# Kernel optimization log

Hardware: AMD Instinct MI355X
Metric: run time of the kernel (lower is better)

## Reference

```python
import jax, jax.numpy as jnp
import numpy as np

DIM = 1024
HEADS = 16
HEAD_DIM = DIM // HEADS
NEG = -1e30
EPS = 1e-5


def _linear(x, w, b):
    # torch nn.Linear: y = x @ W^T + b, W: [out, in]
    return jnp.einsum('bnd,od->bno', x, w) + b


def _mha(x, ctx, wq, bq, wk, bk, wv, bv, wo, bo, mask):
    B, N, D = x.shape
    M = ctx.shape[1]
    q = _linear(x, wq, bq).reshape(B, N, HEADS, HEAD_DIM).transpose(0, 2, 1, 3)
    k = _linear(ctx, wk, bk).reshape(B, M, HEADS, HEAD_DIM).transpose(0, 2, 1, 3)
    v = _linear(ctx, wv, bv).reshape(B, M, HEADS, HEAD_DIM).transpose(0, 2, 1, 3)
    scores = jnp.einsum('bhqd,bhkd->bhqk', q, k) / np.sqrt(HEAD_DIM).astype(np.float32)
    if mask is not None:
        scores = jnp.where(mask == 0, NEG, scores)
    attn = jax.nn.softmax(scores, axis=-1)  # dropout = identity (eval mode)
    out = jnp.einsum('bhqk,bhkd->bhqd', attn, v)
    out = out.transpose(0, 2, 1, 3).reshape(B, N, D)
    return _linear(out, wo, bo)


def _ln(x, g, b):
    mu = jnp.mean(x, axis=-1, keepdims=True)
    var = jnp.mean(jnp.square(x - mu), axis=-1, keepdims=True)
    return (x - mu) * jax.lax.rsqrt(var + EPS) * g + b


def setup_inputs() -> dict:
    key = jax.random.key(0)
    ks = jax.random.split(key, 24)
    B, N, M = 2, 2048, 1024
    s = 0.02
    d = {
        'x': jax.random.normal(ks[0], (B, N, DIM), jnp.float32),
        'memory': jax.random.normal(ks[1], (B, M, DIM), jnp.float32),
        'mask': jnp.tril(jnp.ones((N, N), jnp.int32))[None, None],
    }
    i = 2
    for p in ['sa', 'ca']:
        for nm in ['q', 'k', 'v', 'o']:
            d[f'{p}_w{nm}'] = jax.random.normal(ks[i], (DIM, DIM), jnp.float32) * s; i += 1
            d[f'{p}_b{nm}'] = jnp.zeros((DIM,), jnp.float32)
    d['ff_w1'] = jax.random.normal(ks[i], (4 * DIM, DIM), jnp.float32) * s; i += 1
    d['ff_b1'] = jnp.zeros((4 * DIM,), jnp.float32)
    d['ff_w2'] = jax.random.normal(ks[i], (DIM, 4 * DIM), jnp.float32) * s; i += 1
    d['ff_b2'] = jnp.zeros((DIM,), jnp.float32)
    for j in (1, 2, 3):
        d[f'ln{j}_g'] = jnp.ones((DIM,), jnp.float32)
        d[f'ln{j}_b'] = jnp.zeros((DIM,), jnp.float32)
    return d


def reference(x, memory, mask,
              sa_wq, sa_bq, sa_wk, sa_bk, sa_wv, sa_bv, sa_wo, sa_bo,
              ca_wq, ca_bq, ca_wk, ca_bk, ca_wv, ca_bv, ca_wo, ca_bo,
              ff_w1, ff_b1, ff_w2, ff_b2,
              ln1_g, ln1_b, ln2_g, ln2_b, ln3_g, ln3_b):
    x = _ln(x + _mha(x, x, sa_wq, sa_bq, sa_wk, sa_bk, sa_wv, sa_bv, sa_wo, sa_bo, mask), ln1_g, ln1_b)
    x = _ln(x + _mha(x, memory, ca_wq, ca_bq, ca_wk, ca_bk, ca_wv, ca_bv, ca_wo, ca_bo, None), ln2_g, ln2_b)
    h = jax.nn.relu(_linear(x, ff_w1, ff_b1))  # dropout = identity (eval)
    x = _ln(x + _linear(h, ff_w2, ff_b2), ln3_g, ln3_b)
    return x
```

## Files before the change

### kernel.cpp

```cpp
#include <hip/hip_runtime.h>


typedef __attribute__((ext_vector_type(8))) short bf16x8;
typedef __attribute__((ext_vector_type(4))) float f32x4;

__device__ __forceinline__ unsigned short f2bf(float f) {
    union { float f; unsigned int u; } v; v.f = f;
    unsigned int r = v.u + 0x7fffu + ((v.u >> 16) & 1u);
    return (unsigned short)(r >> 16);
}
__device__ __forceinline__ float bf2f(unsigned short u) {
    union { unsigned int u; float f; } v; v.u = (unsigned int)u << 16;
    return v.f;
}
__device__ __forceinline__ unsigned int bftrunc(float f) {
    union { float f; unsigned int u; } v; v.f = f;
    return v.u >> 16;
}

struct ConvArgs {
    const float* src[12];
    unsigned short* dst[12];
    int blk_ofs[13];
    int n4[12];
    const float* bq; const float* bk; const float* bv;
    const float* ck; const float* cv;
    float* bqkv; float* bkvc;
};
__global__ __launch_bounds__(256) void conv_multi(ConvArgs a)
{
    int bid = blockIdx.x;
    if (bid >= a.blk_ofs[12]) {
        int i = (bid - a.blk_ofs[12]) * 256 + threadIdx.x;
        if (i < 1024)       a.bqkv[i] = a.bq[i];
        else if (i < 2048)  a.bqkv[i] = a.bk[i - 1024];
        else if (i < 3072)  a.bqkv[i] = a.bv[i - 2048];
        else if (i < 4096)  a.bkvc[i - 3072] = a.ck[i - 3072];
        else if (i < 5120)  a.bkvc[i - 3072] = a.cv[i - 4096];
        return;
    }
    int s = 0;
#pragma unroll
    for (int t = 0; t < 12; ++t) if (bid >= a.blk_ofs[t + 1]) s = t + 1;
    int i = (bid - a.blk_ofs[s]) * 256 + threadIdx.x;
    if (i >= a.n4[s]) return;
    float4 v = ((const float4*)a.src[s])[i];
    ushort4 o;
    o.x = f2bf(v.x); o.y = f2bf(v.y); o.z = f2bf(v.z); o.w = f2bf(v.w);
    ((ushort4*)a.dst[s])[i] = o;
}

template<int TM, int TN, int EPI, int SK>
__device__ __forceinline__ void gemm_body(
    unsigned short (*As)[64], unsigned short (*Bs)[64],
    const unsigned short* __restrict__ A, const unsigned short* __restrict__ W,
    const float* __restrict__ bias, unsigned short* __restrict__ out,
    int K, int Ncols, long slice_stride, int bid, int gx, int zslice)
{
    constexpr int AI = TM / 32;
    constexpr int BJ = TN / 32;

    const int tid  = threadIdx.x;
    const int lane = tid & 63;
    const int wave = tid >> 6;
    const int qd   = lane >> 4;
    const int l15  = lane & 15;
    const int wm   = (wave >> 1) * (TM / 2);
    const int wn   = (wave & 1) * (TN / 2);

    const int gpg = 8 * gx;
    const long m0 = (long)((bid / gpg) * 8 + (bid & 7)) * TM;
    const long n0 = (long)((bid % gpg) >> 3) * TN;

    f32x4 acc[AI][BJ] = {};

    const int srow = lane >> 3;
    const int scol = (((lane & 7) ^ srow)) * 8;
    const unsigned short* Ag = A + (m0 + wave * (8 * AI) + srow) * (long)K + scol;
    const unsigned short* Wg = W + (n0 + wave * (8 * BJ) + srow) * (long)K + scol;

    const int ksl   = K / SK;
    const int kbase = (SK > 1) ? zslice * ksl : 0;

    for (int k0 = kbase; k0 < kbase + ksl; k0 += 64) {
#pragma unroll
        for (int c = 0; c < AI; ++c)
            __builtin_amdgcn_global_load_lds(
                (const __attribute__((address_space(1))) unsigned int*)(Ag + (long)c * 8 * K + k0),
                (__attribute__((address_space(3))) unsigned int*)((char*)&As[0][0] + (wave * AI + c) * 1024),
                16, 0, 0);
#pragma unroll
        for (int c = 0; c < BJ; ++c)
            __builtin_amdgcn_global_load_lds(
                (const __attribute__((address_space(1))) unsigned int*)(Wg + (long)c * 8 * K + k0),
                (__attribute__((address_space(3))) unsigned int*)((char*)&Bs[0][0] + (wave * BJ + c) * 1024),
                16, 0, 0);
        __syncthreads();
#pragma unroll
        for (int kk = 0; kk < 64; kk += 32) {
            const int pg = ((((kk >> 3) + qd)) ^ (l15 & 7)) * 8;
            bf16x8 af[AI], bw[BJ];
#pragma unroll
            for (int i = 0; i < AI; ++i)
                af[i] = *(const bf16x8*)&As[wm + i * 16 + l15][pg];
#pragma unroll
            for (int j = 0; j < BJ; ++j)
                bw[j] = *(const bf16x8*)&Bs[wn + j * 16 + l15][pg];
#pragma unroll
            for (int i = 0; i < AI; ++i)
#pragma unroll
                for (int j = 0; j < BJ; ++j)
                    acc[i][j] = __builtin_amdgcn_mfma_f32_16x16x32_bf16(
                        af[i], bw[j], acc[i][j], 0, 0, 0);
        }
        __syncthreads();
    }

    unsigned short* op = out + ((SK > 1) ? (long)zslice * slice_stride : 0);
#pragma unroll
    for (int j = 0; j < BJ; ++j) {
        long col = n0 + wn + j * 16 + l15;
        float bv = (SK == 1 || zslice == 0) ? bias[col] : 0.f;
#pragma unroll
        for (int i = 0; i < AI; ++i) {
#pragma unroll
            for (int r = 0; r < 4; ++r) {
                long row = m0 + wm + i * 16 + qd * 4 + r;
                float v = acc[i][j][r] + bv;
                if (EPI == 1) v = (v > 0.f) ? v : 0.f;
                op[row * Ncols + col] = f2bf(v);
            }
        }
    }
}

template<int TM, int TN, int EPI, int SK>
__global__ __launch_bounds__(256) void gemm_bt(
    const unsigned short* __restrict__ A, const unsigned short* __restrict__ W,
    const float* __restrict__ bias, unsigned short* __restrict__ out,
    int K, int Ncols, long slice_stride)
{
    __shared__ unsigned short As[TM][64];
    __shared__ unsigned short Bs[TN][64];
    const int bid = blockIdx.y * gridDim.x + blockIdx.x;
    gemm_body<TM, TN, EPI, SK>(As, Bs, A, W, bias, out, K, Ncols, slice_stride,
                               bid, gridDim.x, (int)blockIdx.z);
}

template<int EPI, int SK>
__device__ __forceinline__ void gemm8_body(
    unsigned short* Ab, unsigned short* Bb,
    const unsigned short* __restrict__ A, const unsigned short* __restrict__ W,
    const float* __restrict__ bias, unsigned short* __restrict__ out,
    int K, int Ncols, long slice_stride, int mb, int nb, int zslice)
{
    const int tid  = threadIdx.x;
    const int lane = tid & 63;
    const int wave = tid >> 6;
    const int qd   = lane >> 4;
    const int l15  = lane & 15;
    const int wm   = (wave >> 2) * 128;
    const int wn   = (wave & 3) * 64;

    const long m0 = (long)mb * 256;
    const long n0 = (long)nb * 256;

    const int ksl   = K / SK;
    const int kbase = (SK > 1) ? zslice * ksl : 0;
    const int NG    = ksl / 64;

    f32x4 acc[8][4] = {};

    const int srow = tid >> 3;
    const int sgrp = ((tid & 7) ^ (srow & 7)) * 8;
    const unsigned short* Ag = A + (m0 + srow) * (long)K + kbase + sgrp;
    const unsigned short* Wg = W + (n0 + srow) * (long)K + kbase + sgrp;

    auto stA = [&](int db, int r0, int kt) {
        __builtin_amdgcn_global_load_lds(
            (const __attribute__((address_space(1))) unsigned int*)(Ag + (long)r0 * K + kt * 64),
            (__attribute__((address_space(3))) unsigned int*)(Ab + db * 16384 + r0 * 64 + wave * 512),
            16, 0, 0);
    };
    auto stB = [&](int db, int r0, int kt) {
        __builtin_amdgcn_global_load_lds(
            (const __attribute__((address_space(1))) unsigned int*)(Wg + (long)r0 * K + kt * 64),
            (__attribute__((address_space(3))) unsigned int*)(Bb + db * 16384 + r0 * 64 + wave * 512),
            16, 0, 0);
    };
    auto rdA = [&](int db, int row, int kk) -> bf16x8 {
        const int p = (((kk << 2) + qd) ^ (l15 & 7)) << 3;
        return *(const bf16x8*)(Ab + db * 16384 + row * 64 + p);
    };
    auto rdB = [&](int db, int row, int kk) -> bf16x8 {
        const int p = (((kk << 2) + qd) ^ (l15 & 7)) << 3;
        return *(const bf16x8*)(Bb + db * 16384 + row * 64 + p);
    };

#pragma unroll
    for (int h = 0; h < 4; ++h) stA(0, h * 64, 0);
#pragma unroll
    for (int h = 0; h < 4; ++h) stB(0, h * 64, 0);
    if (NG > 1) {
#pragma unroll
        for (int h = 0; h < 4; ++h) stB(1, h * 64, 1);
        stA(1, 0, 1); stA(1, 128, 1);
        asm volatile("s_waitcnt vmcnt(6)" ::: "memory");
    } else {
        asm volatile("s_waitcnt vmcnt(0)" ::: "memory");
    }
    __builtin_amdgcn_s_barrier();

    for (int g = 0; g < NG; ++g) {
        const int db = g & 1, ob = db ^ 1;
        bf16x8 af[4][2], bw[4][2];

        if (g + 1 < NG) { stA(ob, 64, g + 1); stA(ob, 192, g + 1); }

#pragma unroll
        for (int i = 0; i < 4; ++i)
#pragma unroll
            for (int kk = 0; kk < 2; ++kk)
                af[i][kk] = rdA(db, wm + i * 16 + l15, kk);
#pragma unroll
        for (int j = 0; j < 4; ++j)
#pragma unroll
            for (int kk = 0; kk < 2; ++kk)
                bw[j][kk] = rdB(db, wn + j * 16 + l15, kk);
        __builtin_amdgcn_s_setprio(1);
#pragma unroll
        for (int i = 0; i < 4; ++i)
#pragma unroll
            for (int j = 0; j < 4; ++j) {
                acc[i][j] = __builtin_amdgcn_mfma_f32_16x16x32_bf16(af[i][0], bw[j][0], acc[i][j], 0, 0, 0);
                acc[i][j] = __builtin_amdgcn_mfma_f32_16x16x32_bf16(af[i][1], bw[j][1], acc[i][j], 0, 0, 0);
            }
        __builtin_amdgcn_s_setprio(0);
        __builtin_amdgcn_s_barrier();

        if (g + 2 < NG) {
#pragma unroll
            for (int h = 0; h < 4; ++h) stB(db, h * 64, g + 2);
            stA(db, 0, g + 2); stA(db, 128, g + 2);
        }

#pragma unroll
        for (int i = 0; i < 4; ++i)
#pragma unroll
            for (int kk = 0; kk < 2; ++kk)
                af[i][kk] = rdA(db, wm + 64 + i * 16 + l15, kk);
        __builtin_amdgcn_s_setprio(1);
#pragma unroll
        for (int i = 0; i < 4; ++i)
#pragma unroll
            for (int j = 0; j < 4; ++j) {
                acc[4 + i][j] = __builtin_amdgcn_mfma_f32_16x16x32_bf16(af[i][0], bw[j][0], acc[4 + i][j], 0, 0, 0);
                acc[4 + i][j] = __builtin_amdgcn_mfma_f32_16x16x32_bf16(af[i][1], bw[j][1], acc[4 + i][j], 0, 0, 0);
            }
        __builtin_amdgcn_s_setprio(0);

        if (g + 2 < NG)      { asm volatile("s_waitcnt vmcnt(6)" ::: "memory"); }
        else if (g + 1 < NG) { asm volatile("s_waitcnt vmcnt(0)" ::: "memory"); }
        __builtin_amdgcn_s_barrier();
    }

    unsigned short* op = out + ((SK > 1) ? (long)zslice * slice_stride : 0);
#pragma unroll
    for (int j = 0; j < 4; ++j) {
        long col = n0 + wn + j * 16 + l15;
        float bv = (SK == 1 || zslice == 0) ? bias[col] : 0.f;
#pragma unroll
        for (int i = 0; i < 8; ++i) {
#pragma unroll
            for (int r = 0; r < 4; ++r) {
                long row = m0 + wm + (i >> 2) * 64 + (i & 3) * 16 + qd * 4 + r;
                float v = acc[i][j][r] + bv;
                if (EPI == 1) v = (v > 0.f) ? v : 0.f;
                op[row * Ncols + col] = f2bf(v);
            }
        }
    }
}

template<int EPI, int SK, int MODE>
__global__ __launch_bounds__(512) void gemm8_bt(
    const unsigned short* __restrict__ A, const unsigned short* __restrict__ W,
    const float* __restrict__ bias, unsigned short* __restrict__ out,
    int K, int Ncols, long slice_stride)
{
    extern __shared__ unsigned short smem[];
    const int bid = blockIdx.x;
    const int x = bid & 7;
    const int s = bid >> 3;
    int mb, nb, z = 0;
    if (MODE == 1) {
        mb = (x >> 1) * 4 + (s & 3);
        nb = (x & 1) * 8 + (s >> 2);
    } else {
        z  = x >> 1;
        mb = (x & 1) * 8 + (s & 7);
        nb = s >> 3;
    }
    gemm8_body<EPI, SK>(smem, smem + 32768, A, W, bias, out, K, Ncols,
                        slice_stride, mb, nb, z);
}

__global__ __launch_bounds__(512) void gemm8_dual(
    const unsigned short* A0, const unsigned short* W0, const float* b0,
    unsigned short* o0, int K0, int N0,
    const unsigned short* A1, const unsigned short* W1, const float* b1,
    unsigned short* o1, int K1, int N1)
{
    extern __shared__ unsigned short smem[];
    const int bid = blockIdx.x;
    const int x = bid & 7;
    const int s = bid >> 3;
    if (s < 24) {
        const int mb = (x >> 1) * 4 + (s & 3);
        const int nb = (x & 1) * 6 + (s >> 2);
        gemm8_body<0, 1>(smem, smem + 32768, A0, W0, b0, o0, K0, N0, 0, mb, nb, 0);
    } else {
        const int t = s - 24;
        const int mb = (x >> 1) * 2 + (t & 1);
        const int nb = (x & 1) * 4 + (t >> 1);
        gemm8_body<0, 1>(smem, smem + 32768, A1, W1, b1, o1, K1, N1, 0, mb, nb, 0);
    }
}

__global__ __launch_bounds__(256) void attn_kernel(
    const unsigned short* __restrict__ Qb, int q_stride,
    const unsigned short* __restrict__ KVb, int kv_stride, int koff, int voff,
    unsigned short* __restrict__ O,
    int Nq, int Mk, int causal)
{
    __shared__ unsigned short Ks[64][64];
    __shared__ unsigned short Vs[64][64];
    __shared__ unsigned short Ps[4][16][64];

    const int tid  = threadIdx.x;
    const int lane = tid & 63;
    const int wave = tid >> 6;
    const int qd   = lane >> 4;
    const int l15  = lane & 15;
    const int l7   = l15 & 7;
    const int h    = blockIdx.y;
    const int b    = blockIdx.z;
    int jq = blockIdx.x;
    if (causal && (b & 1)) jq = gridDim.x - 1 - jq;
    const int q0 = jq * 64;
    const int tb = q0 + wave * 16;

    bf16x8 aq0, aq1;
    {
        const unsigned short* qp =
            Qb + (long)(b * Nq + tb + l15) * q_stride + h * 64 + qd * 8;
        aq0 = *(const bf16x8*)qp;
        aq1 = *(const bf16x8*)(qp + 32);
    }

    float lpart[4] = {};
    f32x4 oacc[4] = {};

    const int krow  = tid >> 3;
    const int kcol  = (tid & 7) * 8;
    const int kcolS = (((tid & 7) ^ (krow & 7))) * 8;
    const int vj   = tid & 31;
    const int va_k = (vj & 15) + ((vj & 16) << 1);
    const int vfg  = (tid >> 5) * 8;
    const int vpc  = (va_k & 15) * 4 + (va_k >> 4);

    const unsigned short* Kg = KVb + (long)b * Mk * kv_stride + koff + h * 64;
    const unsigned short* Vg = KVb + (long)b * Mk * kv_stride + voff + h * 64;

    bf16x8 kr0, kr1, vra, vrb;
    auto prefetch = [&](int k0) {
        kr0 = *(const bf16x8*)(Kg + (long)(k0 + krow) * kv_stride + kcol);
        kr1 = *(const bf16x8*)(Kg + (long)(k0 + krow + 32) * kv_stride + kcol);
        const unsigned short* v0 = Vg + (long)(k0 + va_k) * kv_stride + vfg;
        vra = *(const bf16x8*)v0;
        vrb = *(const bf16x8*)(v0 + 16 * kv_stride);
    };

    const int nk = causal ? (q0 + 64) : Mk;
    prefetch(0);
    const float SCL = 0.125f * 1.44269504f;

    for (int k0 = 0; k0 < nk; k0 += 64) {
        __syncthreads();
        *(bf16x8*)&Ks[krow][kcolS]      = kr0;
        *(bf16x8*)&Ks[krow + 32][kcolS] = kr1;
#pragma unroll
        for (int jf = 0; jf < 8; ++jf) {
            unsigned int d = (unsigned short)vra[jf] |
                             ((unsigned int)(unsigned short)vrb[jf] << 16);
            const int row = vfg + jf;
            *(unsigned int*)&Vs[row][vpc ^ ((row & 7) << 3)] = d;
        }
        if (k0 + 64 < nk) prefetch(k0 + 64);
        __syncthreads();

        if (!causal || (k0 <= tb + 15)) {
            bf16x8 bk[4][2];
#pragma unroll
            for (int kt = 0; kt < 4; ++kt)
#pragma unroll
                for (int c = 0; c < 2; ++c)
                    bk[kt][c] = *(const bf16x8*)&Ks[kt * 16 + l15][((c * 4 + qd) ^ l7) * 8];
            f32x4 s[4];
#pragma unroll
            for (int kt = 0; kt < 4; ++kt) {
                f32x4 z = {};
                z = __builtin_amdgcn_mfma_f32_16x16x32_bf16(aq0, bk[kt][0], z, 0, 0, 0);
                z = __builtin_amdgcn_mfma_f32_16x16x32_bf16(aq1, bk[kt][1], z, 0, 0, 0);
                s[kt] = z;
            }
            const bool needmask = causal && (k0 + 63 > tb);
#pragma unroll
            for (int r = 0; r < 4; ++r) {
                const int qg = tb + qd * 4 + r;
                float e[4];
#pragma unroll
                for (int kt = 0; kt < 4; ++kt) {
                    float ev = __builtin_amdgcn_exp2f(s[kt][r] * SCL);
                    if (needmask && (k0 + kt * 16 + l15 > qg)) ev = 0.f;
                    e[kt] = ev;
                }
                lpart[r] += (e[0] + e[1]) + (e[2] + e[3]);
                unsigned int lo = bftrunc(e[0]) | (bftrunc(e[1]) << 16);
                unsigned int hi = bftrunc(e[2]) | (bftrunc(e[3]) << 16);
                uint2 pk; pk.x = lo; pk.y = hi;
                const int prow = qd * 4 + r;
                *(uint2*)&Ps[wave][prow][(l15 * 4) ^ ((prow & 7) << 3)] = pk;
            }
            bf16x8 bv[4][2];
#pragma unroll
            for (int dt = 0; dt < 4; ++dt)
#pragma unroll
                for (int c = 0; c < 2; ++c)
                    bv[dt][c] = *(const bf16x8*)&Vs[dt * 16 + l15][((c * 4 + qd) ^ l7) * 8];
            bf16x8 ap0 = *(const bf16x8*)&Ps[wave][l15][(qd ^ l7) * 8];
            bf16x8 ap1 = *(const bf16x8*)&Ps[wave][l15][((4 + qd) ^ l7) * 8];
#pragma unroll
            for (int dt = 0; dt < 4; ++dt) {
                oacc[dt] = __builtin_amdgcn_mfma_f32_16x16x32_bf16(
                    ap0, bv[dt][0], oacc[dt], 0, 0, 0);
                oacc[dt] = __builtin_amdgcn_mfma_f32_16x16x32_bf16(
                    ap1, bv[dt][1], oacc[dt], 0, 0, 0);
            }
        }
    }

#pragma unroll
    for (int r = 0; r < 4; ++r) {
        float l = lpart[r];
        l += __shfl_xor(l, 1);
        l += __shfl_xor(l, 2);
        l += __shfl_xor(l, 4);
        l += __shfl_xor(l, 8);
        float inv = 1.f / l;
        long row = (long)(b * Nq + tb + qd * 4 + r);
#pragma unroll
        for (int dt = 0; dt < 4; ++dt)
            O[row * 1024 + h * 64 + dt * 16 + l15] = f2bf(oacc[dt][r] * inv);
    }
}

template<int ND, int RESBF>
__global__ __launch_bounds__(256) void ln_res_kernel(
    const void* __restrict__ res, const unsigned short* __restrict__ delta,
    long dstride, const float* __restrict__ g, const float* __restrict__ beta,
    float* __restrict__ yout, unsigned short* __restrict__ ybf)
{
    __shared__ float red[8];
    const int row = blockIdx.x;
    const int tid = threadIdx.x;
    const long base = (long)row * 1024 + tid * 4;
    float v0, v1, v2, v3;
    if (RESBF) {
        ushort4 a = *(const ushort4*)((const unsigned short*)res + base);
        v0 = bf2f(a.x); v1 = bf2f(a.y); v2 = bf2f(a.z); v3 = bf2f(a.w);
    } else {
        float4 a = *(const float4*)((const float*)res + base);
        v0 = a.x; v1 = a.y; v2 = a.z; v3 = a.w;
    }
#pragma unroll
    for (int t = 0; t < ND; ++t) {
        ushort4 d = *(const ushort4*)(delta + t * dstride + base);
        v0 += bf2f(d.x); v1 += bf2f(d.y); v2 += bf2f(d.z); v3 += bf2f(d.w);
    }
    float s  = v0 + v1 + v2 + v3;
    float ss = v0 * v0 + v1 * v1 + v2 * v2 + v3 * v3;
#pragma unroll
    for (int off = 1; off < 64; off <<= 1) {
        s  += __shfl_xor(s, off);
        ss += __shfl_xor(ss, off);
    }
    const int wave = tid >> 6;
    if ((tid & 63) == 0) { red[wave] = s; red[4 + wave] = ss; }
    __syncthreads();
    float st  = red[0] + red[1] + red[2] + red[3];
    float sst = red[4] + red[5] + red[6] + red[7];
    float mean = st * (1.f / 1024.f);
    float var  = sst * (1.f / 1024.f) - mean * mean;
    float inv  = rsqrtf(var + 1e-5f);
    const int c = tid * 4;
    float y0 = (v0 - mean) * inv * g[c + 0] + beta[c + 0];
    float y1 = (v1 - mean) * inv * g[c + 1] + beta[c + 1];
    float y2 = (v2 - mean) * inv * g[c + 2] + beta[c + 2];
    float y3 = (v3 - mean) * inv * g[c + 3] + beta[c + 3];
    if (yout) *(float4*)(yout + base) = make_float4(y0, y1, y2, y3);
    if (ybf) {
        ushort4 o;
        o.x = f2bf(y0); o.y = f2bf(y1); o.z = f2bf(y2); o.w = f2bf(y3);
        *(ushort4*)(ybf + base) = o;
    }
}

extern "C" void kernel_launch(void* const* d_in, const int* in_sizes, int n_in,
                              void* d_out, int out_size, void* d_ws, size_t ws_size,
                              hipStream_t stream)
{
    const int B = 2, N = 2048, M = 1024, D = 1024, FF = 4096;
    const int TN = B * N;
    const int TM = B * M;
    const size_t MB = 1024 * 1024;

    const float* x     = (const float*)d_in[0];
    const float* mem   = (const float*)d_in[1];
    const float* sa_wq = (const float*)d_in[3];  const float* sa_bq = (const float*)d_in[4];
    const float* sa_wk = (const float*)d_in[5];  const float* sa_bk = (const float*)d_in[6];
    const float* sa_wv = (const float*)d_in[7];  const float* sa_bv = (const float*)d_in[8];
    const float* sa_wo = (const float*)d_in[9];  const float* sa_bo = (const float*)d_in[10];
    const float* ca_wq = (const float*)d_in[11]; const float* ca_bq = (const float*)d_in[12];
    const float* ca_wk = (const float*)d_in[13]; const float* ca_bk = (const float*)d_in[14];
    const float* ca_wv = (const float*)d_in[15]; const float* ca_bv = (const float*)d_in[16];
    const float* ca_wo = (const float*)d_in[17]; const float* ca_bo = (const float*)d_in[18];
    const float* ff_w1 = (const float*)d_in[19]; const float* ff_b1 = (const float*)d_in[20];
    const float* ff_w2 = (const float*)d_in[21]; const float* ff_b2 = (const float*)d_in[22];
    const float* ln1_g = (const float*)d_in[23]; const float* ln1_b = (const float*)d_in[24];
    const float* ln2_g = (const float*)d_in[25]; const float* ln2_b = (const float*)d_in[26];
    const float* ln3_g = (const float*)d_in[27]; const float* ln3_b = (const float*)d_in[28];

    char* w = (char*)d_ws;
    size_t off = 0;
    auto alloc = [&](size_t bytes) -> char* {
        char* p = w + off; off += (bytes + 255) & ~(size_t)255; return p;
    };

    unsigned short* xb   = (unsigned short*)alloc((size_t)TN * D * 2);
    unsigned short* memb = (unsigned short*)alloc((size_t)TM * D * 2);
    unsigned short* wqkv = (unsigned short*)alloc((size_t)3 * D * D * 2);
    unsigned short* wos  = (unsigned short*)alloc((size_t)D * D * 2);
    unsigned short* wqc  = (unsigned short*)alloc((size_t)D * D * 2);
    unsigned short* wkvc = (unsigned short*)alloc((size_t)2 * D * D * 2);
    unsigned short* woc  = (unsigned short*)alloc((size_t)D * D * 2);
    unsigned short* w1b  = (unsigned short*)alloc((size_t)FF * D * 2);
    unsigned short* w2b  = (unsigned short*)alloc((size_t)D * FF * 2);
    char* big = alloc((size_t)80 * MB);
    unsigned short* qkv   = (unsigned short*)big;
    unsigned short* ab    = (unsigned short*)(big + 24 * MB);
    unsigned short* kvb   = (unsigned short*)(big + 32 * MB);
    unsigned short* qb    = (unsigned short*)(big + 40 * MB);
    unsigned short* hb    = (unsigned short*)big;
    unsigned short* tmpbf = (unsigned short*)(big + 48 * MB);
    const long      TSL   = (long)TN * D;
    float* bqkv = (float*)alloc((size_t)3 * D * 4);
    float* bkvc = (float*)alloc((size_t)2 * D * 4);

    ConvArgs ca;
    const float* srcs[12] = {x, mem, sa_wq, sa_wk, sa_wv, sa_wo,
                             ca_wq, ca_wk, ca_wv, ca_wo, ff_w1, ff_w2};
    unsigned short* dsts[12] = {xb, memb, wqkv, wqkv + (size_t)D * D,
                                wqkv + (size_t)2 * D * D, wos, wqc, wkvc,
                                wkvc + (size_t)D * D, woc, w1b, w2b};
    long ns[12] = {(long)TN * D, (long)TM * D, (long)D * D, (long)D * D,
                   (long)D * D, (long)D * D, (long)D * D, (long)D * D,
                   (long)D * D, (long)D * D, (long)FF * D, (long)D * FF};
    int total_blk = 0;
    for (int i = 0; i < 12; ++i) {
        ca.src[i] = srcs[i]; ca.dst[i] = dsts[i];
        ca.n4[i] = (int)(ns[i] / 4);
        ca.blk_ofs[i] = total_blk;
        total_blk += (ca.n4[i] + 255) / 256;
    }
    ca.blk_ofs[12] = total_blk;
    ca.bq = sa_bq; ca.bk = sa_bk; ca.bv = sa_bv; ca.ck = ca_bk; ca.cv = ca_bv;
    ca.bqkv = bqkv; ca.bkvc = bkvc;
    conv_multi<<<dim3(total_blk + 20), dim3(256), 0, stream>>>(ca);

    dim3 blk(256);
    dim3 blk8(512);
    const unsigned int LDS8 = 131072;

    gemm8_dual<<<dim3(256), blk8, LDS8, stream>>>(
        xb,   wqkv, bqkv, qkv, D, 3 * D,
        memb, wkvc, bkvc, kvb, D, 2 * D);

    attn_kernel<<<dim3(N / 64, 16, B), blk, 0, stream>>>(
        qkv, 3 * D, qkv, 3 * D, D, 2 * D, ab, N, N, 1);
    gemm_bt<128, 64, 0, 2><<<dim3(D / 64, TN / 128, 2), blk, 0, stream>>>(
        ab, wos, sa_bo, tmpbf, D, D, TSL);
    ln_res_kernel<2, 0><<<dim3(TN), blk, 0, stream>>>(
        x, tmpbf, TSL, ln1_g, ln1_b, nullptr, xb);

    gemm_bt<128, 64, 0, 1><<<dim3(D / 64, TN / 128), blk, 0, stream>>>(
        xb, wqc, ca_bq, qb, D, D, 0);
    attn_kernel<<<dim3(N / 64, 16, B), blk, 0, stream>>>(
        qb, D, kvb, 2 * D, 0, D, ab, N, M, 0);
    gemm_bt<128, 64, 0, 2><<<dim3(D / 64, TN / 128, 2), blk, 0, stream>>>(
        ab, woc, ca_bo, tmpbf, D, D, TSL);
    ln_res_kernel<2, 1><<<dim3(TN), blk, 0, stream>>>(
        xb, tmpbf, TSL, ln2_g, ln2_b, nullptr, xb);

    gemm8_bt<1, 1, 1><<<dim3(256), blk8, LDS8, stream>>>(
        xb, w1b, ff_b1, hb, D, FF, 0);
    gemm8_bt<0, 4, 2><<<dim3(256), blk8, LDS8, stream>>>(
        hb, w2b, ff_b2, tmpbf, FF, D, TSL);
    ln_res_kernel<4, 1><<<dim3(TN), blk, 0, stream>>>(
        xb, tmpbf, TSL, ln3_g, ln3_b, (float*)d_out, nullptr);
}
```

Measured before the change: 455.5 us.

## Enlarge attention query tile to 128 rows with 8 waves and split K/V loader roles

The attention kernel now processes 128 query rows per block with 512 threads, so each K/V tile loaded into shared memory is reused by twice as many waves. Loading is split so half the threads fetch V and half fetch K. The V transpose uses byte-permute instructions. The softmax scale is folded into Q once at load time, which removes a multiply per score but adds bf16 rounding of the scaled Q. The P bf16 packing switches to a perm-based truncation. Risks are fewer blocks (lower occupancy and parallelism), and more causal-mask waste in diagonal tiles since waves now scan up to q0+128.

```diff
diff --git a/kernel.cpp b/kernel.cpp
--- a/kernel.cpp
+++ b/kernel.cpp
@@ -13,9 +13,9 @@
     union { unsigned int u; float f; } v; v.u = (unsigned int)u << 16;
     return v.f;
 }
-__device__ __forceinline__ unsigned int bftrunc(float f) {
+__device__ __forceinline__ unsigned int fbits(float f) {
     union { float f; unsigned int u; } v; v.f = f;
-    return v.u >> 16;
+    return v.u;
 }
 
 struct ConvArgs {
@@ -327,7 +327,7 @@
     }
 }
 
-__global__ __launch_bounds__(256) void attn_kernel(
+__global__ __launch_bounds__(512) void attn_kernel(
     const unsigned short* __restrict__ Qb, int q_stride,
     const unsigned short* __restrict__ KVb, int kv_stride, int koff, int voff,
     unsigned short* __restrict__ O,
@@ -335,7 +335,7 @@
 {
     __shared__ unsigned short Ks[64][64];
     __shared__ unsigned short Vs[64][64];
-    __shared__ unsigned short Ps[4][16][64];
+    __shared__ unsigned short Ps[8][16][64];
 
     const int tid  = threadIdx.x;
     const int lane = tid & 63;
@@ -347,8 +347,10 @@
     const int b    = blockIdx.z;
     int jq = blockIdx.x;
     if (causal && (b & 1)) jq = gridDim.x - 1 - jq;
-    const int q0 = jq * 64;
+    const int q0 = jq * 128;
     const int tb = q0 + wave * 16;
+
+    const float SCL = 0.125f * 1.44269504f;
 
     bf16x8 aq0, aq1;
     {
@@ -356,45 +358,60 @@
             Qb + (long)(b * Nq + tb + l15) * q_stride + h * 64 + qd * 8;
         aq0 = *(const bf16x8*)qp;
         aq1 = *(const bf16x8*)(qp + 32);
+#pragma unroll
+        for (int j = 0; j < 8; ++j) {
+            aq0[j] = (short)f2bf(bf2f((unsigned short)aq0[j]) * SCL);
+            aq1[j] = (short)f2bf(bf2f((unsigned short)aq1[j]) * SCL);
+        }
     }
 
     float lpart[4] = {};
     f32x4 oacc[4] = {};
 
-    const int krow  = tid >> 3;
-    const int kcol  = (tid & 7) * 8;
-    const int kcolS = (((tid & 7) ^ (krow & 7))) * 8;
-    const int vj   = tid & 31;
+    const bool vrole = (tid < 256);
+    const int vt   = tid & 255;
+    const int vj   = vt & 31;
     const int va_k = (vj & 15) + ((vj & 16) << 1);
-    const int vfg  = (tid >> 5) * 8;
+    const int vfg  = (vt >> 5) * 8;
     const int vpc  = (va_k & 15) * 4 + (va_k >> 4);
+    const int krow  = vt >> 3;
+    const int kcol  = (vt & 7) * 8;
+    const int kcolS = (((vt & 7) ^ (krow & 7))) * 8;
 
     const unsigned short* Kg = KVb + (long)b * Mk * kv_stride + koff + h * 64;
     const unsigned short* Vg = KVb + (long)b * Mk * kv_stride + voff + h * 64;
 
-    bf16x8 kr0, kr1, vra, vrb;
+    bf16x8 r0, r1;
     auto prefetch = [&](int k0) {
-        kr0 = *(const bf16x8*)(Kg + (long)(k0 + krow) * kv_stride + kcol);
-        kr1 = *(const bf16x8*)(Kg + (long)(k0 + krow + 32) * kv_stride + kcol);
-        const unsigned short* v0 = Vg + (long)(k0 + va_k) * kv_stride + vfg;
-        vra = *(const bf16x8*)v0;
-        vrb = *(const bf16x8*)(v0 + 16 * kv_stride);
+        if (vrole) {
+            const unsigned short* v0 = Vg + (long)(k0 + va_k) * kv_stride + vfg;
+            r0 = *(const bf16x8*)v0;
+            r1 = *(const bf16x8*)(v0 + 16 * kv_stride);
+        } else {
+            r0 = *(const bf16x8*)(Kg + (long)(k0 + krow) * kv_stride + kcol);
+            r1 = *(const bf16x8*)(Kg + (long)(k0 + krow + 32) * kv_stride + kcol);
+        }
     };
 
-    const int nk = causal ? (q0 + 64) : Mk;
+    const int nk = causal ? (q0 + 128) : Mk;
     prefetch(0);
-    const float SCL = 0.125f * 1.44269504f;
 
     for (int k0 = 0; k0 < nk; k0 += 64) {
         __syncthreads();
-        *(bf16x8*)&Ks[krow][kcolS]      = kr0;
-        *(bf16x8*)&Ks[krow + 32][kcolS] = kr1;
-#pragma unroll
-        for (int jf = 0; jf < 8; ++jf) {
-            unsigned int d = (unsigned short)vra[jf] |
-                             ((unsigned int)(unsigned short)vrb[jf] << 16);
-            const int row = vfg + jf;
-            *(unsigned int*)&Vs[row][vpc ^ ((row & 7) << 3)] = d;
+        if (vrole) {
+            const unsigned int* pa = (const unsigned int*)&r0;
+            const unsigned int* pb = (const unsigned int*)&r1;
+#pragma unroll
+            for (int w2 = 0; w2 < 4; ++w2) {
+                unsigned int d0 = __builtin_amdgcn_perm(pb[w2], pa[w2], 0x05040100u);
+                unsigned int d1 = __builtin_amdgcn_perm(pb[w2], pa[w2], 0x07060302u);
+                const int rr0 = vfg + 2 * w2, rr1 = rr0 + 1;
+                *(unsigned int*)&Vs[rr0][vpc ^ ((rr0 & 7) << 3)] = d0;
+                *(unsigned int*)&Vs[rr1][vpc ^ ((rr1 & 7) << 3)] = d1;
+            }
+        } else {
+            *(bf16x8*)&Ks[krow][kcolS]      = r0;
+            *(bf16x8*)&Ks[krow + 32][kcolS] = r1;
         }
         if (k0 + 64 < nk) prefetch(k0 + 64);
         __syncthreads();
@@ -421,13 +438,13 @@
                 float e[4];
 #pragma unroll
                 for (int kt = 0; kt < 4; ++kt) {
-                    float ev = __builtin_amdgcn_exp2f(s[kt][r] * SCL);
+                    float ev = __builtin_amdgcn_exp2f(s[kt][r]);
                     if (needmask && (k0 + kt * 16 + l15 > qg)) ev = 0.f;
                     e[kt] = ev;
                 }
                 lpart[r] += (e[0] + e[1]) + (e[2] + e[3]);
-                unsigned int lo = bftrunc(e[0]) | (bftrunc(e[1]) << 16);
-                unsigned int hi = bftrunc(e[2]) | (bftrunc(e[3]) << 16);
+                unsigned int lo = __builtin_amdgcn_perm(fbits(e[1]), fbits(e[0]), 0x07060302u);
+                unsigned int hi = __builtin_amdgcn_perm(fbits(e[3]), fbits(e[2]), 0x07060302u);
                 uint2 pk; pk.x = lo; pk.y = hi;
                 const int prow = qd * 4 + r;
                 *(uint2*)&Ps[wave][prow][(l15 * 4) ^ ((prow & 7) << 3)] = pk;
@@ -596,7 +613,7 @@
         xb,   wqkv, bqkv, qkv, D, 3 * D,
         memb, wkvc, bkvc, kvb, D, 2 * D);
 
-    attn_kernel<<<dim3(N / 64, 16, B), blk, 0, stream>>>(
+    attn_kernel<<<dim3(N / 128, 16, B), blk8, 0, stream>>>(
         qkv, 3 * D, qkv, 3 * D, D, 2 * D, ab, N, N, 1);
     gemm_bt<128, 64, 0, 2><<<dim3(D / 64, TN / 128, 2), blk, 0, stream>>>(
         ab, wos, sa_bo, tmpbf, D, D, TSL);
@@ -605,7 +622,7 @@
 
     gemm_bt<128, 64, 0, 1><<<dim3(D / 64, TN / 128), blk, 0, stream>>>(
         xb, wqc, ca_bq, qb, D, D, 0);
-    attn_kernel<<<dim3(N / 64, 16, B), blk, 0, stream>>>(
+    attn_kernel<<<dim3(N / 128, 16, B), blk8, 0, stream>>>(
         qb, D, kvb, 2 * D, 0, D, ab, N, M, 0);
     gemm_bt<128, 64, 0, 2><<<dim3(D / 64, TN / 128, 2), blk, 0, stream>>>(
         ab, woc, ca_bo, tmpbf, D, D, TSL);
```

New measurement: 464.4 us. No clear change (+2.0%).
